# Optimization experiments

Measured on AMD Instinct MI355X. Metric: run time of the kernel, lower is better.

Reference implementation:

```python
import jax, jax.numpy as jnp
import numpy as np

N_S, N_T, E, B = 100000, 100000, 2000000, 10000
F_XS, F_XT, F_E, F_U = 10, 5, 10, 10


def setup_inputs() -> dict:
    key = jax.random.key(0)
    ks = jax.random.split(key, 8)
    return {
        "x_s": jax.random.normal(ks[0], (N_S, F_XS), dtype=jnp.float32),
        "x_t": jax.random.normal(ks[1], (N_T, F_XT), dtype=jnp.float32),
        "edge_index": jax.random.randint(ks[2], (2, E), 0, N_S),
        "edge_attr": jax.random.normal(ks[3], (E, F_E), dtype=jnp.float32),
        "u": jax.random.normal(ks[4], (B, F_U), dtype=jnp.float32),
        "batch_e": jax.random.randint(ks[5], (E,), 0, B),
        "W1": jax.random.normal(ks[6], (F_XS + F_XT + F_E + F_U, F_E), dtype=jnp.float32) * (1.0 / np.sqrt(F_XS + F_XT + F_E + F_U)),
        "b1": jnp.zeros((F_E,), dtype=jnp.float32),
        "W2": jax.random.normal(ks[7], (F_E, F_E), dtype=jnp.float32) * (1.0 / np.sqrt(F_E)),
        "b2": jnp.zeros((F_E,), dtype=jnp.float32),
    }


def reference(x_s, x_t, edge_index, edge_attr, u, batch_e, W1, b1, W2, b2):
    src, tgt = edge_index[0], edge_index[1]
    # Gather + concat: [E, F_xs + F_xt + F_e + F_u]
    h = jnp.concatenate([x_s[src], x_t[tgt], edge_attr, u[batch_e]], axis=-1)
    h = jax.nn.leaky_relu(h @ W1 + b1, negative_slope=0.1)
    return h @ W2 + b2  # [E, F_e]
```

## Files before the change

### kernel.cpp

```cpp
#include <hip/hip_runtime.h>


#define F_XS 10
#define F_XT 5
#define F_E  10
#define F_U  10
#define F_IN 35

typedef float vf4 __attribute__((ext_vector_type(4)));
typedef float vf2 __attribute__((ext_vector_type(2)));
typedef _Float16 f16;

__global__ __launch_bounds__(256) void convert_tables_kernel(
    const float* __restrict__ xs, const float* __restrict__ xt, const float* __restrict__ uu,
    f16* __restrict__ xs_h, f16* __restrict__ xt_h, f16* __restrict__ u_h,
    int n_xs_elems, int n_u_elems, int n_t_rows)
{
    const int tid = blockIdx.x * blockDim.x + threadIdx.x;
    if (tid < n_xs_elems) {
        xs_h[tid] = (f16)xs[tid];
    } else if (tid < n_xs_elems + n_u_elems) {
        const int i = tid - n_xs_elems;
        u_h[i] = (f16)uu[i];
    } else {
        const int r = tid - n_xs_elems - n_u_elems;
        if (r < n_t_rows) {
            const float* p = xt + (long long)r * F_XT;
            f16* q = xt_h + (long long)r * 6;
            #pragma unroll
            for (int i = 0; i < 5; ++i) q[i] = (f16)p[i];
            q[5] = (f16)0.f;
        }
    }
}

__global__ __launch_bounds__(256) void edge_model_f16tab_kernel(
    const f16*   __restrict__ xs_h,
    const f16*   __restrict__ xt_h,
    const int*   __restrict__ edge_index,
    const float* __restrict__ edge_attr,
    const f16*   __restrict__ u_h,
    const int*   __restrict__ batch_e,
    const float* __restrict__ W1,
    const float* __restrict__ b1,
    const float* __restrict__ W2,
    const float* __restrict__ b2,
    float*       __restrict__ out,
    int E)
{
    const int e = blockIdx.x * blockDim.x + threadIdx.x;
    if (e >= E) return;

    const int src = __builtin_nontemporal_load(edge_index + e);
    const int tgt = __builtin_nontemporal_load(edge_index + E + e);
    const int be  = __builtin_nontemporal_load(batch_e + e);

    f16 s[10];  __builtin_memcpy(s, xs_h + (long long)src * 10, 20);
    f16 t[8];   __builtin_memcpy(t, xt_h + (long long)tgt * 6, 16);
    f16 uv[10]; __builtin_memcpy(uv, u_h + (long long)be * 10, 20);

    const float* pe = edge_attr + (long long)e * F_E;
    vf4 a0 = __builtin_nontemporal_load((const vf4*)(pe));
    vf4 a1 = __builtin_nontemporal_load((const vf4*)(pe + 4));
    vf2 a2 = __builtin_nontemporal_load((const vf2*)(pe + 8));

    float h[F_E];
    #pragma unroll
    for (int j = 0; j < F_E; ++j) h[j] = b1[j];

    #pragma unroll
    for (int k = 0; k < 10; ++k) {
        const float a = (float)s[k];
        #pragma unroll
        for (int j = 0; j < F_E; ++j) h[j] = fmaf(a, W1[k * F_E + j], h[j]);
    }
    #pragma unroll
    for (int k = 0; k < 5; ++k) {
        const float a = (float)t[k];
        #pragma unroll
        for (int j = 0; j < F_E; ++j) h[j] = fmaf(a, W1[(10 + k) * F_E + j], h[j]);
    }
    {
        float seg[10] = {a0.x,a0.y,a0.z,a0.w, a1.x,a1.y,a1.z,a1.w, a2.x,a2.y};
        #pragma unroll
        for (int k = 0; k < 10; ++k) {
            #pragma unroll
            for (int j = 0; j < F_E; ++j) h[j] = fmaf(seg[k], W1[(15 + k) * F_E + j], h[j]);
        }
    }
    #pragma unroll
    for (int k = 0; k < 10; ++k) {
        const float a = (float)uv[k];
        #pragma unroll
        for (int j = 0; j < F_E; ++j) h[j] = fmaf(a, W1[(25 + k) * F_E + j], h[j]);
    }

    #pragma unroll
    for (int j = 0; j < F_E; ++j) h[j] = (h[j] >= 0.0f) ? h[j] : 0.1f * h[j];

    float o[F_E];
    #pragma unroll
    for (int j = 0; j < F_E; ++j) o[j] = b2[j];
    #pragma unroll
    for (int k = 0; k < F_E; ++k) {
        const float a = h[k];
        #pragma unroll
        for (int j = 0; j < F_E; ++j) o[j] = fmaf(a, W2[k * F_E + j], o[j]);
    }

    float* po = out + (long long)e * F_E;
    vf4 w0; w0.x=o[0]; w0.y=o[1]; w0.z=o[2]; w0.w=o[3];
    vf4 w1; w1.x=o[4]; w1.y=o[5]; w1.z=o[6]; w1.w=o[7];
    vf2 w2; w2.x=o[8]; w2.y=o[9];
    *(vf4*)(po)     = w0;
    *(vf4*)(po + 4) = w1;
    *(vf2*)(po + 8) = w2;
}

__global__ __launch_bounds__(256) void edge_model_f32_kernel(
    const float* __restrict__ x_s, const float* __restrict__ x_t,
    const int*   __restrict__ edge_index, const float* __restrict__ edge_attr,
    const float* __restrict__ u, const int* __restrict__ batch_e,
    const float* __restrict__ W1, const float* __restrict__ b1,
    const float* __restrict__ W2, const float* __restrict__ b2,
    float* __restrict__ out, int E)
{
    const int e = blockIdx.x * blockDim.x + threadIdx.x;
    if (e >= E) return;
    const int src = __builtin_nontemporal_load(edge_index + e);
    const int tgt = __builtin_nontemporal_load(edge_index + E + e);
    const int be  = __builtin_nontemporal_load(batch_e + e);

    float in[F_IN];
    __builtin_memcpy(in,      x_s + (long long)src * F_XS, 40);
    __builtin_memcpy(in + 10, x_t + (long long)tgt * F_XT, 20);
    const float* pe = edge_attr + (long long)e * F_E;
    vf4 a0 = __builtin_nontemporal_load((const vf4*)(pe));
    vf4 a1 = __builtin_nontemporal_load((const vf4*)(pe + 4));
    vf2 a2 = __builtin_nontemporal_load((const vf2*)(pe + 8));
    in[15]=a0.x; in[16]=a0.y; in[17]=a0.z; in[18]=a0.w;
    in[19]=a1.x; in[20]=a1.y; in[21]=a1.z; in[22]=a1.w;
    in[23]=a2.x; in[24]=a2.y;
    __builtin_memcpy(in + 25, u + (long long)be * F_U, 40);

    float h[F_E];
    #pragma unroll
    for (int j = 0; j < F_E; ++j) h[j] = b1[j];
    #pragma unroll
    for (int k = 0; k < F_IN; ++k) {
        const float a = in[k];
        #pragma unroll
        for (int j = 0; j < F_E; ++j) h[j] = fmaf(a, W1[k * F_E + j], h[j]);
    }
    #pragma unroll
    for (int j = 0; j < F_E; ++j) h[j] = (h[j] >= 0.0f) ? h[j] : 0.1f * h[j];

    float o[F_E];
    #pragma unroll
    for (int j = 0; j < F_E; ++j) o[j] = b2[j];
    #pragma unroll
    for (int k = 0; k < F_E; ++k) {
        const float a = h[k];
        #pragma unroll
        for (int j = 0; j < F_E; ++j) o[j] = fmaf(a, W2[k * F_E + j], o[j]);
    }
    float* po = out + (long long)e * F_E;
    vf4 w0; w0.x=o[0]; w0.y=o[1]; w0.z=o[2]; w0.w=o[3];
    vf4 w1; w1.x=o[4]; w1.y=o[5]; w1.z=o[6]; w1.w=o[7];
    vf2 w2; w2.x=o[8]; w2.y=o[9];
    *(vf4*)(po)     = w0;
    *(vf4*)(po + 4) = w1;
    *(vf2*)(po + 8) = w2;
}

extern "C" void kernel_launch(void* const* d_in, const int* in_sizes, int n_in,
                              void* d_out, int out_size, void* d_ws, size_t ws_size,
                              hipStream_t stream) {
    const float* x_s        = (const float*)d_in[0];
    const float* x_t        = (const float*)d_in[1];
    const int*   edge_index = (const int*)  d_in[2];
    const float* edge_attr  = (const float*)d_in[3];
    const float* u          = (const float*)d_in[4];
    const int*   batch_e    = (const int*)  d_in[5];
    const float* W1         = (const float*)d_in[6];
    const float* b1         = (const float*)d_in[7];
    const float* W2         = (const float*)d_in[8];
    const float* b2         = (const float*)d_in[9];
    float*       out        = (float*)d_out;

    const int E   = in_sizes[5];
    const int N_S = in_sizes[0] / F_XS;
    const int N_T = in_sizes[1] / F_XT;
    const int Bn  = in_sizes[4] / F_U;

    const size_t xs_bytes = (size_t)N_S * 10 * sizeof(f16);
    const size_t xs_off   = 0;
    const size_t xt_off   = (xs_off + xs_bytes + 15) & ~(size_t)15;
    const size_t xt_bytes = (size_t)N_T * 6 * sizeof(f16) + 16;
    const size_t u_off    = (xt_off + xt_bytes + 15) & ~(size_t)15;
    const size_t u_bytes  = (size_t)Bn * 10 * sizeof(f16);
    const size_t need     = u_off + u_bytes;

    const int block = 256;
    const int grid_e = (E + block - 1) / block;

    if (ws_size >= need) {
        f16* xs_h = (f16*)((char*)d_ws + xs_off);
        f16* xt_h = (f16*)((char*)d_ws + xt_off);
        f16* u_h  = (f16*)((char*)d_ws + u_off);

        const int n_xs = N_S * 10, n_u = Bn * 10;
        const int conv_threads = n_xs + n_u + N_T;
        convert_tables_kernel<<<(conv_threads + block - 1) / block, block, 0, stream>>>(
            x_s, x_t, u, xs_h, xt_h, u_h, n_xs, n_u, N_T);

        edge_model_f16tab_kernel<<<grid_e, block, 0, stream>>>(
            xs_h, xt_h, edge_index, edge_attr, u_h, batch_e, W1, b1, W2, b2, out, E);
    } else {
        edge_model_f32_kernel<<<grid_e, block, 0, stream>>>(
            x_s, x_t, edge_index, edge_attr, u, batch_e, W1, b1, W2, b2, out, E);
    }
}
```

Measured before the change: 239.6 us.

## Process four edges per thread with vectorized index, attribute and output access

```diff
diff --git a/kernel.cpp b/kernel.cpp
--- a/kernel.cpp
+++ b/kernel.cpp
@@ -6,9 +6,11 @@
 #define F_E  10
 #define F_U  10
 #define F_IN 35
+#define EPT  4
 
 typedef float vf4 __attribute__((ext_vector_type(4)));
 typedef float vf2 __attribute__((ext_vector_type(2)));
+typedef int   vi4 __attribute__((ext_vector_type(4)));
 typedef _Float16 f16;
 
 __global__ __launch_bounds__(256) void convert_tables_kernel(
@@ -34,7 +36,56 @@
     }
 }
 
-__global__ __launch_bounds__(256) void edge_model_f16tab_kernel(
+__device__ __forceinline__ void compute_edge(
+    const f16* __restrict__ s, const f16* __restrict__ t, const f16* __restrict__ uv,
+    const float* __restrict__ a,
+    const float* __restrict__ W1, const float* __restrict__ b1,
+    const float* __restrict__ W2, const float* __restrict__ b2,
+    float* __restrict__ o)
+{
+    float h[F_E];
+    #pragma unroll
+    for (int j = 0; j < F_E; ++j) h[j] = b1[j];
+
+    #pragma unroll
+    for (int k = 0; k < 10; ++k) {
+        const float x = (float)s[k];
+        #pragma unroll
+        for (int j = 0; j < F_E; ++j) h[j] = fmaf(x, W1[k * F_E + j], h[j]);
+    }
+    #pragma unroll
+    for (int k = 0; k < 5; ++k) {
+        const float x = (float)t[k];
+        #pragma unroll
+        for (int j = 0; j < F_E; ++j) h[j] = fmaf(x, W1[(10 + k) * F_E + j], h[j]);
+    }
+    #pragma unroll
+    for (int k = 0; k < 10; ++k) {
+        const float x = a[k];
+        #pragma unroll
+        for (int j = 0; j < F_E; ++j) h[j] = fmaf(x, W1[(15 + k) * F_E + j], h[j]);
+    }
+    #pragma unroll
+    for (int k = 0; k < 10; ++k) {
+        const float x = (float)uv[k];
+        #pragma unroll
+        for (int j = 0; j < F_E; ++j) h[j] = fmaf(x, W1[(25 + k) * F_E + j], h[j]);
+    }
+
+    #pragma unroll
+    for (int j = 0; j < F_E; ++j) h[j] = (h[j] >= 0.0f) ? h[j] : 0.1f * h[j];
+
+    #pragma unroll
+    for (int j = 0; j < F_E; ++j) o[j] = b2[j];
+    #pragma unroll
+    for (int k = 0; k < F_E; ++k) {
+        const float x = h[k];
+        #pragma unroll
+        for (int j = 0; j < F_E; ++j) o[j] = fmaf(x, W2[k * F_E + j], o[j]);
+    }
+}
+
+__global__ __launch_bounds__(256) void edge_model_f16tab_ept4_kernel(
     const f16*   __restrict__ xs_h,
     const f16*   __restrict__ xt_h,
     const int*   __restrict__ edge_index,
@@ -48,6 +99,80 @@
     float*       __restrict__ out,
     int E)
 {
+    const long long base =
+        ((long long)blockIdx.x * blockDim.x + threadIdx.x) * (long long)EPT;
+    if (base >= E) return;
+
+    if (base + EPT <= E) {
+        const vi4 srcs = __builtin_nontemporal_load((const vi4*)(edge_index + base));
+        const vi4 tgts = __builtin_nontemporal_load((const vi4*)(edge_index + E + base));
+        const vi4 bes  = __builtin_nontemporal_load((const vi4*)(batch_e + base));
+
+        f16 s[EPT][10];
+        f16 tt[EPT][8];
+        f16 uv[EPT][10];
+        #pragma unroll
+        for (int i = 0; i < EPT; ++i) {
+            const int src = srcs[i];
+            const int tgt = tgts[i];
+            const int be  = bes[i];
+            __builtin_memcpy(s[i],  xs_h + (long long)src * 10, 20);
+            __builtin_memcpy(tt[i], xt_h + (long long)tgt * 6, 16);
+            __builtin_memcpy(uv[i], u_h  + (long long)be  * 10, 20);
+        }
+
+        const vf4* pa = (const vf4*)(edge_attr + base * F_E);
+        float af[4 * F_E];
+        #pragma unroll
+        for (int q = 0; q < 10; ++q) {
+            const vf4 v = __builtin_nontemporal_load(pa + q);
+            af[4 * q + 0] = v.x; af[4 * q + 1] = v.y;
+            af[4 * q + 2] = v.z; af[4 * q + 3] = v.w;
+        }
+
+        float of[4 * F_E];
+        #pragma unroll
+        for (int i = 0; i < EPT; ++i)
+            compute_edge(s[i], tt[i], uv[i], af + F_E * i, W1, b1, W2, b2, of + F_E * i);
+
+        vf4* po = (vf4*)(out + base * F_E);
+        #pragma unroll
+        for (int q = 0; q < 10; ++q) {
+            vf4 v;
+            v.x = of[4 * q + 0]; v.y = of[4 * q + 1];
+            v.z = of[4 * q + 2]; v.w = of[4 * q + 3];
+            po[q] = v;
+        }
+    } else {
+        for (int i = 0; i < EPT; ++i) {
+            const long long e = base + i;
+            if (e >= E) break;
+            const int src = edge_index[e];
+            const int tgt = edge_index[E + e];
+            const int be  = batch_e[e];
+            f16 s1[10], t1[8], u1[10];
+            __builtin_memcpy(s1, xs_h + (long long)src * 10, 20);
+            __builtin_memcpy(t1, xt_h + (long long)tgt * 6, 16);
+            __builtin_memcpy(u1, u_h  + (long long)be  * 10, 20);
+            float a1[F_E];
+            #pragma unroll
+            for (int k = 0; k < F_E; ++k) a1[k] = edge_attr[e * F_E + k];
+            float o1[F_E];
+            compute_edge(s1, t1, u1, a1, W1, b1, W2, b2, o1);
+            #pragma unroll
+            for (int j = 0; j < F_E; ++j) out[e * F_E + j] = o1[j];
+        }
+    }
+}
+
+__global__ __launch_bounds__(256) void edge_model_f16tab_kernel(
+    const f16*   __restrict__ xs_h, const f16* __restrict__ xt_h,
+    const int*   __restrict__ edge_index, const float* __restrict__ edge_attr,
+    const f16*   __restrict__ u_h, const int* __restrict__ batch_e,
+    const float* __restrict__ W1, const float* __restrict__ b1,
+    const float* __restrict__ W2, const float* __restrict__ b2,
+    float* __restrict__ out, int E)
+{
     const int e = blockIdx.x * blockDim.x + threadIdx.x;
     if (e >= E) return;
 
@@ -63,50 +188,10 @@
     vf4 a0 = __builtin_nontemporal_load((const vf4*)(pe));
     vf4 a1 = __builtin_nontemporal_load((const vf4*)(pe + 4));
     vf2 a2 = __builtin_nontemporal_load((const vf2*)(pe + 8));
-
-    float h[F_E];
-    #pragma unroll
-    for (int j = 0; j < F_E; ++j) h[j] = b1[j];
-
-    #pragma unroll
-    for (int k = 0; k < 10; ++k) {
-        const float a = (float)s[k];
-        #pragma unroll
-        for (int j = 0; j < F_E; ++j) h[j] = fmaf(a, W1[k * F_E + j], h[j]);
-    }
-    #pragma unroll
-    for (int k = 0; k < 5; ++k) {
-        const float a = (float)t[k];
-        #pragma unroll
-        for (int j = 0; j < F_E; ++j) h[j] = fmaf(a, W1[(10 + k) * F_E + j], h[j]);
-    }
-    {
-        float seg[10] = {a0.x,a0.y,a0.z,a0.w, a1.x,a1.y,a1.z,a1.w, a2.x,a2.y};
-        #pragma unroll
-        for (int k = 0; k < 10; ++k) {
-            #pragma unroll
-            for (int j = 0; j < F_E; ++j) h[j] = fmaf(seg[k], W1[(15 + k) * F_E + j], h[j]);
-        }
-    }
-    #pragma unroll
-    for (int k = 0; k < 10; ++k) {
-        const float a = (float)uv[k];
-        #pragma unroll
-        for (int j = 0; j < F_E; ++j) h[j] = fmaf(a, W1[(25 + k) * F_E + j], h[j]);
-    }
-
-    #pragma unroll
-    for (int j = 0; j < F_E; ++j) h[j] = (h[j] >= 0.0f) ? h[j] : 0.1f * h[j];
+    float af[F_E] = {a0.x,a0.y,a0.z,a0.w, a1.x,a1.y,a1.z,a1.w, a2.x,a2.y};
 
     float o[F_E];
-    #pragma unroll
-    for (int j = 0; j < F_E; ++j) o[j] = b2[j];
-    #pragma unroll
-    for (int k = 0; k < F_E; ++k) {
-        const float a = h[k];
-        #pragma unroll
-        for (int j = 0; j < F_E; ++j) o[j] = fmaf(a, W2[k * F_E + j], o[j]);
-    }
+    compute_edge(s, t, uv, af, W1, b1, W2, b2, o);
 
     float* po = out + (long long)e * F_E;
     vf4 w0; w0.x=o[0]; w0.y=o[1]; w0.z=o[2]; w0.w=o[3];
@@ -202,7 +287,6 @@
     const size_t need     = u_off + u_bytes;
 
     const int block = 256;
-    const int grid_e = (E + block - 1) / block;
 
     if (ws_size >= need) {
         f16* xs_h = (f16*)((char*)d_ws + xs_off);
@@ -214,9 +298,18 @@
         convert_tables_kernel<<<(conv_threads + block - 1) / block, block, 0, stream>>>(
             x_s, x_t, u, xs_h, xt_h, u_h, n_xs, n_u, N_T);
 
-        edge_model_f16tab_kernel<<<grid_e, block, 0, stream>>>(
-            xs_h, xt_h, edge_index, edge_attr, u_h, batch_e, W1, b1, W2, b2, out, E);
+        if ((E & 3) == 0) {
+            const int edges_per_block = block * EPT;
+            const int grid_e = (E + edges_per_block - 1) / edges_per_block;
+            edge_model_f16tab_ept4_kernel<<<grid_e, block, 0, stream>>>(
+                xs_h, xt_h, edge_index, edge_attr, u_h, batch_e, W1, b1, W2, b2, out, E);
+        } else {
+            const int grid_e = (E + block - 1) / block;
+            edge_model_f16tab_kernel<<<grid_e, block, 0, stream>>>(
+                xs_h, xt_h, edge_index, edge_attr, u_h, batch_e, W1, b1, W2, b2, out, E);
+        }
     } else {
+        const int grid_e = (E + block - 1) / block;
         edge_model_f32_kernel<<<grid_e, block, 0, stream>>>(
             x_s, x_t, edge_index, edge_attr, u, batch_e, W1, b1, W2, b2, out, E);
     }
```

Result: slower. 288.1 us (+20.3%).
